# Performance work log

Hardware: AMD Instinct MI355X
Metric: run time of the kernel (lower is better)

The kernel has to match this reference:

```python
import math
import jax, jax.numpy as jnp
import numpy as np

TWO_PI = 2.0 * math.pi

def ring_pe(s, K):
    # s: [N] in [0,1). Returns [N, 2K]: interleaved cos/sin harmonics k=1..K.
    k = jnp.arange(1, K + 1, dtype=s.dtype)            # [K]
    ang = TWO_PI * s[:, None] * k[None, :]             # [N, K]
    pe = jnp.stack([jnp.cos(ang), jnp.sin(ang)], axis=-1)  # [N, K, 2]
    return pe.reshape(s.shape[0], 2 * K)

def setup_inputs() -> dict:
    key = jax.random.key(0)
    k1, k2, k3, k4 = jax.random.split(key, 4)
    N, Z, H, K = 2048, 32, 64, 2
    in_dim = 2 * (2 * K) + 2 + Z  # 42
    return {
        "z_g": jax.random.normal(k1, (1, Z), dtype=jnp.float32),
        "s": jax.random.uniform(k2, (N,), dtype=jnp.float32),
        "W1": jax.random.normal(k3, (in_dim, H), dtype=jnp.float32) * (1.0 / math.sqrt(in_dim)),
        "b1": jnp.zeros((H,), dtype=jnp.float32),
        "W2": jax.random.normal(k4, (H, 1), dtype=jnp.float32) * (1.0 / math.sqrt(H)),
        "b2": jnp.zeros((1,), dtype=jnp.float32),
        "K": K,
    }

def reference(z_g, s, W1, b1, W2, b2, K):
    N = s.shape[0]
    pe = ring_pe(s, K)                                  # [N, 2K]
    pe_i = jnp.broadcast_to(pe[:, None, :], (N, N, pe.shape[-1]))
    pe_j = jnp.broadcast_to(pe[None, :, :], (N, N, pe.shape[-1]))
    diff = s[:, None] - s[None, :]
    diff = diff - jnp.floor(diff)
    diff = jnp.minimum(diff, 1.0 - diff)                # circular distance in [0, 0.5]
    diff_pe = jnp.stack([jnp.cos(TWO_PI * diff), jnp.sin(TWO_PI * diff)], axis=-1)  # [N, N, 2]
    zrep = jnp.broadcast_to(z_g.reshape(1, 1, -1), (N, N, z_g.shape[-1]))
    x = jnp.concatenate([pe_i, pe_j, diff_pe, zrep], axis=-1)  # [N, N, 42]
    h = jax.nn.relu(jnp.einsum('ijd,dh->ijh', x, W1) + b1)
    logits = (jnp.einsum('ijh,ho->ijo', h, W2) + b2)[..., 0]   # [N, N]
    logits = 0.5 * (logits + logits.T)
    eye = jnp.eye(N, dtype=bool)
    return jnp.where(eye, jnp.float32(-1e9), logits)
```

## Files before the change

### kernel.cpp

```cpp
#include <hip/hip_runtime.h>
#include <math.h>

#define TWO_PI_F 6.28318530717958647692f

typedef unsigned int u32;
typedef __attribute__((ext_vector_type(4))) float    f4;
typedef __attribute__((ext_vector_type(16))) float   f16v;
typedef __attribute__((ext_vector_type(2))) float    f2;
typedef __attribute__((ext_vector_type(2))) _Float16 h2;
typedef __attribute__((ext_vector_type(4))) _Float16 h4;
typedef __attribute__((ext_vector_type(8))) _Float16 h8;

union B8 { h8 v; h4 q[2]; };
union C2 { u32 w[2]; h4 v; };
union P4 { h2 a[4]; h8 v; };

#if __has_builtin(__builtin_amdgcn_fdot2)
#define FDOT2(a, b, c) __builtin_amdgcn_fdot2((a), (b), (c), false)
#else
__device__ __forceinline__ float FDOT2(h2 a, h2 b, float c) {
    return c + (float)a[0] * (float)b[0] + (float)a[1] * (float)b[1];
}
#endif

#if __has_builtin(__builtin_amdgcn_cvt_pkrtz)
__device__ __forceinline__ h2 CVTPK(float a, float b) {
    return __builtin_bit_cast(h2, __builtin_amdgcn_cvt_pkrtz(a, b));
}
#else
__device__ __forceinline__ h2 CVTPK(float a, float b) {
    return (h2){(_Float16)a, (_Float16)b};
}
#endif

__global__ __launch_bounds__(256, 4) void gd_mfma(
    const float* __restrict__ z,  const float* __restrict__ s,
    const float* __restrict__ W1, const float* __restrict__ b1,
    const float* __restrict__ W2, const float* __restrict__ b2v,
    float* __restrict__ out, int N, int NB)
{
    __shared__ __attribute__((aligned(16))) _Float16 Ald[64][24];
    __shared__ __attribute__((aligned(16))) h4 peb[64];
    __shared__ __attribute__((aligned(16))) h2 P2[1024];
    __shared__ __attribute__((aligned(16))) h2 w2p[32];
    __shared__ __attribute__((aligned(16))) float S[2][32][36];
    __shared__ f2 strig[64];

    int u = blockIdx.x;
    int M = 2 * NB + 1;
    float disc = (float)(M * M - 8 * u);
    int bi = (int)(((float)M - sqrtf(disc)) * 0.5f);
    if (bi < 0) bi = 0;
    if (bi > NB - 1) bi = NB - 1;
    while (bi > 0 && bi * (M - bi) / 2 > u) --bi;
    while ((bi + 1) * (M - (bi + 1)) / 2 <= u) ++bi;
    int bj = bi + (u - bi * (M - bi) / 2);

    int t    = threadIdx.x;
    int lane = t & 63;

    if (t >= 64 && t < 96) {
        int r2 = t - 64;
        w2p[r2] = (h2){(_Float16)(0.5f * W2[2 * r2]),
                       (_Float16)(0.5f * W2[2 * r2 + 1])};
    }
    if (t < 64) {
        int grow = (t < 32) ? (bi * 32 + t) : (bj * 32 + (t - 32));
        float ang = TWO_PI_F * s[grow];
        float c1 = __cosf(ang), s1 = __sinf(ang);
        float c2 = c1 * c1 - s1 * s1, s2 = 2.0f * c1 * s1;
        strig[t] = (f2){c1, s1};
        peb[t]   = (h4){(_Float16)c1, (_Float16)s1, (_Float16)c2, (_Float16)s2};

        float zc = b1[t];
#pragma unroll
        for (int zz = 0; zz < 32; ++zz)
            zc = fmaf(z[zz], W1[(10 + zz) * 64 + t], zc);

        h8 row0, row1;
#pragma unroll
        for (int k = 0; k < 8; ++k) row0[k] = (_Float16)W1[k * 64 + t];
        row1 = (h8)0;
        row1[0] = (_Float16)W1[8 * 64 + t];
        row1[1] = (_Float16)W1[9 * 64 + t];
        row1[2] = (_Float16)zc;
        *(h8*)&Ald[t][0] = row0;
        *(h8*)&Ald[t][8] = row1;
    }
    __syncthreads();

    {
        int base = t * 4;
        int il = base >> 5, j0 = base & 31;
        f2 ci = strig[il];
        P4 pk;
#pragma unroll
        for (int c = 0; c < 4; ++c) {
            f2 cj = strig[32 + j0 + c];
            float ctv = fmaf(ci.x, cj.x, ci.y * cj.y);
            float stv = fabsf(fmaf(ci.y, cj.x, -(ci.x * cj.y)));
            pk.a[c] = CVTPK(ctv, stv);
        }
        *(h8*)&P2[base] = pk.v;
    }

    int n = lane & 31;
    int q = lane >> 5;

    h8 afr[2];
    h2 w2h[2][8];
#pragma unroll
    for (int H = 0; H < 2; ++H) {
        afr[H] = *(const h8*)&Ald[H * 32 + n][q * 8];
#pragma unroll
        for (int e = 0; e < 8; ++e)
            w2h[H][e] = w2p[(e & 1) + 4 * (e >> 1) + 2 * q + 16 * H];
    }
    __syncthreads();

    int wv   = t >> 6;
    int o    = wv >> 1;
    int base = (wv & 1) * 16;

    h4 pe_inv = peb[32 + n];

#pragma unroll
    for (int i = 0; i < 8; ++i) {
        int ilA = base + i;
        int ilB = base + i + 8;

        h4 varA = peb[ilA];
        h4 varB = peb[ilB];
        u32 pwA = *(const u32*)&P2[ilA * 32 + n];
        u32 pwB = *(const u32*)&P2[ilB * 32 + n];

        B8 bA, bB;
        {
            h4 pa = o ? pe_inv : varA;
            h4 pb = o ? varA : pe_inv;
            C2 cc; cc.w[0] = pwA; cc.w[1] = 0x00003C00u;
            bA.q[0] = q ? cc.v : pa;
            bA.q[1] = q ? (h4)0 : pb;
        }
        {
            h4 pa = o ? pe_inv : varB;
            h4 pb = o ? varB : pe_inv;
            C2 cc; cc.w[0] = pwB; cc.w[1] = 0x00003C00u;
            bB.q[0] = q ? cc.v : pa;
            bB.q[1] = q ? (h4)0 : pb;
        }

        f16v a0A = __builtin_amdgcn_mfma_f32_32x32x16_f16(afr[0], bA.v, (f16v)(0.0f), 0, 0, 0);
        f16v a1A = __builtin_amdgcn_mfma_f32_32x32x16_f16(afr[1], bA.v, (f16v)(0.0f), 0, 0, 0);
        f16v a0B = __builtin_amdgcn_mfma_f32_32x32x16_f16(afr[0], bB.v, (f16v)(0.0f), 0, 0, 0);
        f16v a1B = __builtin_amdgcn_mfma_f32_32x32x16_f16(afr[1], bB.v, (f16v)(0.0f), 0, 0, 0);

        float pA0 = 0.f, pA1 = 0.f, pA2 = 0.f, pA3 = 0.f;
        float pB0 = 0.f, pB1 = 0.f, pB2 = 0.f, pB3 = 0.f;
#pragma unroll
        for (int e = 0; e < 8; ++e) {
            h2 mA0 = __builtin_elementwise_max(CVTPK(a0A[2 * e], a0A[2 * e + 1]), (h2)0);
            h2 mA1 = __builtin_elementwise_max(CVTPK(a1A[2 * e], a1A[2 * e + 1]), (h2)0);
            h2 mB0 = __builtin_elementwise_max(CVTPK(a0B[2 * e], a0B[2 * e + 1]), (h2)0);
            h2 mB1 = __builtin_elementwise_max(CVTPK(a1B[2 * e], a1B[2 * e + 1]), (h2)0);
            if (e & 1) {
                pA1 = FDOT2(mA0, w2h[0][e], pA1);
                pA3 = FDOT2(mA1, w2h[1][e], pA3);
                pB1 = FDOT2(mB0, w2h[0][e], pB1);
                pB3 = FDOT2(mB1, w2h[1][e], pB3);
            } else {
                pA0 = FDOT2(mA0, w2h[0][e], pA0);
                pA2 = FDOT2(mA1, w2h[1][e], pA2);
                pB0 = FDOT2(mB0, w2h[0][e], pB0);
                pB2 = FDOT2(mB1, w2h[1][e], pB2);
            }
        }
        float psA = (pA0 + pA1) + (pA2 + pA3);
        float psB = (pB0 + pB1) + (pB2 + pB3);
        psA += __shfl_xor(psA, 32);
        psB += __shfl_xor(psB, 32);
        if (q == 0) {
            S[o][ilA][n] = psA;
            S[o][ilB][n] = psB;
        }
    }
    __syncthreads();

    float b2 = b2v[0];
    {
        int il = t >> 3;
        int j0 = (t & 7) * 4;
        f4 a = *(const f4*)&S[0][il][j0];
        f4 b = *(const f4*)&S[1][il][j0];
        f4 v;
#pragma unroll
        for (int c = 0; c < 4; ++c) {
            float x = a[c] + b[c] + b2;
            if (bi == bj && il == j0 + c) x = -1e9f;
            v[c] = x;
        }
        *(f4*)&out[(size_t)(bi * 32 + il) * N + bj * 32 + j0] = v;

        if (bj > bi) {
            int jl = t >> 3;
            int i0 = (t & 7) * 4;
            f4 m;
#pragma unroll
            for (int c = 0; c < 4; ++c)
                m[c] = S[0][i0 + c][jl] + S[1][i0 + c][jl] + b2;
            *(f4*)&out[(size_t)(bj * 32 + jl) * N + bi * 32 + i0] = m;
        }
    }
}

extern "C" void kernel_launch(void* const* d_in, const int* in_sizes, int n_in,
                              void* d_out, int out_size, void* d_ws, size_t ws_size,
                              hipStream_t stream) {
    const float* z  = (const float*)d_in[0];
    const float* s  = (const float*)d_in[1];
    const float* W1 = (const float*)d_in[2];
    const float* b1 = (const float*)d_in[3];
    const float* W2 = (const float*)d_in[4];
    const float* b2 = (const float*)d_in[5];
    int N = in_sizes[1];

    float* out = (float*)d_out;
    int NB = N / 32;
    int nblk = NB * (NB + 1) / 2;
    gd_mfma<<<nblk, 256, 0, stream>>>(z, s, W1, b1, W2, b2, out, N, NB);
}
```

Measured before the change: 29.01 us.

## Rewrite ReLU as half of value plus absolute value, folding the linear part into an MFMA

Uses relu(x) = 0.5(x + |x|) to split the second layer into two parts. The linear part is folded into a precomputed vector L = W1·W2 and evaluated with one extra MFMA per tile. The nonlinear part becomes fp32 FMAs on |h|, where the abs can be a free source modifier. This replaces the per-pair pack-convert, packed max and fdot2 sequence in the epilogue, cutting VALU work at the cost of 50% more MFMA issues and more registers for fp32 W2 weights. The occupancy hint in the launch bounds is also relaxed, presumably to make room for those extra registers.

```diff
diff --git a/kernel.cpp b/kernel.cpp
--- a/kernel.cpp
+++ b/kernel.cpp
@@ -15,14 +15,6 @@
 union C2 { u32 w[2]; h4 v; };
 union P4 { h2 a[4]; h8 v; };
 
-#if __has_builtin(__builtin_amdgcn_fdot2)
-#define FDOT2(a, b, c) __builtin_amdgcn_fdot2((a), (b), (c), false)
-#else
-__device__ __forceinline__ float FDOT2(h2 a, h2 b, float c) {
-    return c + (float)a[0] * (float)b[0] + (float)a[1] * (float)b[1];
-}
-#endif
-
 #if __has_builtin(__builtin_amdgcn_cvt_pkrtz)
 __device__ __forceinline__ h2 CVTPK(float a, float b) {
     return __builtin_bit_cast(h2, __builtin_amdgcn_cvt_pkrtz(a, b));
@@ -33,7 +25,7 @@
 }
 #endif
 
-__global__ __launch_bounds__(256, 4) void gd_mfma(
+__global__ __launch_bounds__(256) void gd_mfma(
     const float* __restrict__ z,  const float* __restrict__ s,
     const float* __restrict__ W1, const float* __restrict__ b1,
     const float* __restrict__ W2, const float* __restrict__ b2v,
@@ -42,8 +34,9 @@
     __shared__ __attribute__((aligned(16))) _Float16 Ald[64][24];
     __shared__ __attribute__((aligned(16))) h4 peb[64];
     __shared__ __attribute__((aligned(16))) h2 P2[1024];
-    __shared__ __attribute__((aligned(16))) h2 w2p[32];
     __shared__ __attribute__((aligned(16))) float S[2][32][36];
+    __shared__ __attribute__((aligned(16))) float w2f[64];
+    __shared__ __attribute__((aligned(16))) _Float16 Lld[16];
     __shared__ f2 strig[64];
 
     int u = blockIdx.x;
@@ -59,11 +52,6 @@
     int t    = threadIdx.x;
     int lane = t & 63;
 
-    if (t >= 64 && t < 96) {
-        int r2 = t - 64;
-        w2p[r2] = (h2){(_Float16)(0.5f * W2[2 * r2]),
-                       (_Float16)(0.5f * W2[2 * r2 + 1])};
-    }
     if (t < 64) {
         int grow = (t < 32) ? (bi * 32 + t) : (bj * 32 + (t - 32));
         float ang = TWO_PI_F * s[grow];
@@ -71,6 +59,7 @@
         float c2 = c1 * c1 - s1 * s1, s2 = 2.0f * c1 * s1;
         strig[t] = (f2){c1, s1};
         peb[t]   = (h4){(_Float16)c1, (_Float16)s1, (_Float16)c2, (_Float16)s2};
+        w2f[t]   = W2[t];
 
         float zc = b1[t];
 #pragma unroll
@@ -103,20 +92,28 @@
         }
         *(h8*)&P2[base] = pk.v;
     }
+    if (t < 16) {
+        float acc = 0.0f;
+        for (int h = 0; h < 64; ++h)
+            acc = fmaf((float)Ald[h][t], w2f[h], acc);
+        Lld[t] = (_Float16)(0.25f * acc);
+    }
 
     int n = lane & 31;
     int q = lane >> 5;
 
     h8 afr[2];
-    h2 w2h[2][8];
+    float w2v[2][16];
 #pragma unroll
     for (int H = 0; H < 2; ++H) {
         afr[H] = *(const h8*)&Ald[H * 32 + n][q * 8];
 #pragma unroll
-        for (int e = 0; e < 8; ++e)
-            w2h[H][e] = w2p[(e & 1) + 4 * (e >> 1) + 2 * q + 16 * H];
+        for (int e = 0; e < 16; ++e)
+            w2v[H][e] = 0.25f * w2f[(e & 3) + 8 * (e >> 2) + 4 * q + 32 * H];
     }
     __syncthreads();
+
+    h8 afrL = *(const h8*)&Lld[q * 8];
 
     int wv   = t >> 6;
     int o    = wv >> 1;
@@ -152,33 +149,30 @@
 
         f16v a0A = __builtin_amdgcn_mfma_f32_32x32x16_f16(afr[0], bA.v, (f16v)(0.0f), 0, 0, 0);
         f16v a1A = __builtin_amdgcn_mfma_f32_32x32x16_f16(afr[1], bA.v, (f16v)(0.0f), 0, 0, 0);
+        f16v lnA = __builtin_amdgcn_mfma_f32_32x32x16_f16(afrL,   bA.v, (f16v)(0.0f), 0, 0, 0);
         f16v a0B = __builtin_amdgcn_mfma_f32_32x32x16_f16(afr[0], bB.v, (f16v)(0.0f), 0, 0, 0);
         f16v a1B = __builtin_amdgcn_mfma_f32_32x32x16_f16(afr[1], bB.v, (f16v)(0.0f), 0, 0, 0);
-
-        float pA0 = 0.f, pA1 = 0.f, pA2 = 0.f, pA3 = 0.f;
-        float pB0 = 0.f, pB1 = 0.f, pB2 = 0.f, pB3 = 0.f;
+        f16v lnB = __builtin_amdgcn_mfma_f32_32x32x16_f16(afrL,   bB.v, (f16v)(0.0f), 0, 0, 0);
+
+        float cA0 = 0.f, cA1 = 0.f, cA2 = 0.f, cA3 = 0.f;
+        float cB0 = 0.f, cB1 = 0.f, cB2 = 0.f, cB3 = 0.f;
 #pragma unroll
         for (int e = 0; e < 8; ++e) {
-            h2 mA0 = __builtin_elementwise_max(CVTPK(a0A[2 * e], a0A[2 * e + 1]), (h2)0);
-            h2 mA1 = __builtin_elementwise_max(CVTPK(a1A[2 * e], a1A[2 * e + 1]), (h2)0);
-            h2 mB0 = __builtin_elementwise_max(CVTPK(a0B[2 * e], a0B[2 * e + 1]), (h2)0);
-            h2 mB1 = __builtin_elementwise_max(CVTPK(a1B[2 * e], a1B[2 * e + 1]), (h2)0);
-            if (e & 1) {
-                pA1 = FDOT2(mA0, w2h[0][e], pA1);
-                pA3 = FDOT2(mA1, w2h[1][e], pA3);
-                pB1 = FDOT2(mB0, w2h[0][e], pB1);
-                pB3 = FDOT2(mB1, w2h[1][e], pB3);
-            } else {
-                pA0 = FDOT2(mA0, w2h[0][e], pA0);
-                pA2 = FDOT2(mA1, w2h[1][e], pA2);
-                pB0 = FDOT2(mB0, w2h[0][e], pB0);
-                pB2 = FDOT2(mB1, w2h[1][e], pB2);
-            }
-        }
-        float psA = (pA0 + pA1) + (pA2 + pA3);
-        float psB = (pB0 + pB1) + (pB2 + pB3);
+            cA0 = fmaf(fabsf(a0A[e]),     w2v[0][e],     cA0);
+            cA1 = fmaf(fabsf(a0A[e + 8]), w2v[0][e + 8], cA1);
+            cA2 = fmaf(fabsf(a1A[e]),     w2v[1][e],     cA2);
+            cA3 = fmaf(fabsf(a1A[e + 8]), w2v[1][e + 8], cA3);
+            cB0 = fmaf(fabsf(a0B[e]),     w2v[0][e],     cB0);
+            cB1 = fmaf(fabsf(a0B[e + 8]), w2v[0][e + 8], cB1);
+            cB2 = fmaf(fabsf(a1B[e]),     w2v[1][e],     cB2);
+            cB3 = fmaf(fabsf(a1B[e + 8]), w2v[1][e + 8], cB3);
+        }
+        float psA = (cA0 + cA1) + (cA2 + cA3);
+        float psB = (cB0 + cB1) + (cB2 + cB3);
         psA += __shfl_xor(psA, 32);
         psB += __shfl_xor(psB, 32);
+        psA += lnA[0];
+        psB += lnB[0];
         if (q == 0) {
             S[o][ilA][n] = psA;
             S[o][ilB][n] = psB;
```

Result: slower. 40.38 us (+39.2%).
